# Optimization experiments

Hardware: AMD Instinct MI355X
Metric: run time of the kernel (lower is better)

The kernel has to match this reference:

```python
import jax, jax.numpy as jnp
import numpy as np

B, S, D, E = 2, 2048, 1024, 8
H = 2 * D          # hidden_dim = 2*n_embd
A = H // 16        # adapt_dim


def _ln(x, g, b):
    m = x.mean(-1, keepdims=True)
    v = x.var(-1, keepdims=True)
    return (x - m) * jax.lax.rsqrt(v + 1e-5) * g + b


def setup_inputs() -> dict:
    key = jax.random.key(0)
    ks = jax.random.split(key, 16)
    s = 1.0 / np.sqrt(D)        # shared-linear init scale
    sa = s * 0.01               # adapter-linear init scale
    sg = 0.01 / np.sqrt(A)      # expert adapter init scale
    f32 = jnp.float32
    return {
        "x": jax.random.normal(ks[0], (B, S, D), f32),
        "expert_weights": jax.nn.softmax(jax.random.normal(ks[1], (B * S, E), f32), -1),
        "up_w": jax.random.normal(ks[2], (H, D), f32) * s,
        "gate_w": jax.random.normal(ks[3], (H, D), f32) * s,
        "down_w": jax.random.normal(ks[4], (D, H), f32) * s,
        "pre_w": jax.random.normal(ks[5], (A, D), f32) * sa,
        "post_w": jax.random.normal(ks[6], (A, H), f32) * sa,
        "an_g": jnp.ones((A,), f32),
        "an_b": jnp.zeros((A,), f32),
        "adapt_proj_w": jax.random.normal(ks[7], (H, A), f32) * sa,
        "adapter_w": jax.random.normal(ks[8], (E, A, A), f32) * sg,
        "adapter_g": jnp.ones((E, A), f32),
        "adapter_b": jnp.zeros((E, A), f32),
        "expert_proj_w": jax.random.normal(ks[9], (H, A), f32) * sg,
        "output_proj_w": jax.random.normal(ks[10], (D, H), f32) * sg,
    }


def reference(x, expert_weights, up_w, gate_w, down_w, pre_w, post_w, an_g, an_b,
              adapt_proj_w, adapter_w, adapter_g, adapter_b, expert_proj_w, output_proj_w):
    # ---- SharedExpertMLP ----
    up = x @ up_w.T                                  # [B,S,H]
    gate = x @ gate_w.T                              # [B,S,H]
    hidden = jax.nn.silu(gate) * up                  # SwiGLU
    adapt_in = _ln(x @ pre_w.T, an_g, an_b)          # [B,S,A]
    adapt_out = _ln(hidden @ post_w.T, an_g, an_b)   # [B,S,A]
    w = jnp.einsum('bsa,bta->bst', adapt_in, adapt_out)
    w = jax.nn.silu(jnp.clip(w, -5.0, 5.0))          # clamp+SiLU score
    # explicit fp32 bmm as in original autocast-disabled block
    adapt = jnp.einsum('bst,bta->bsa',
                       w.astype(jnp.float32),
                       adapt_in.astype(jnp.float32)).astype(x.dtype)
    hidden = hidden + 0.1 * (adapt @ adapt_proj_w.T)
    shared_out = hidden @ down_w.T                   # [B,S,D] (dropout is identity in eval)

    # ---- per-token expert mixing ----
    xf = x.reshape(-1, x.shape[-1])                  # [N,D], N=B*S
    a = _ln(xf @ pre_w.T, an_g, an_b)                # [N,A]
    h = jnp.einsum('na,eca->nec', a, adapter_w)      # per-expert low-rank adapt [N,E,A]
    h = _ln(h, adapter_g[None], adapter_b[None])
    mixed = jnp.einsum('ne,nea->na', expert_weights, h)   # combine experts [N,A]
    out = (mixed @ expert_proj_w.T) @ output_proj_w.T     # [N,D]
    return shared_out + out.reshape(x.shape)
```

## Files before the change

kernel.cpp:

```cpp
#include <hip/hip_runtime.h>
#include <hip/hip_bf16.h>
#include <math.h>

#define Bq 2
#define Sq 2048
#define Dq 1024
#define Eq 8
#define Hq 2048
#define Aq 128
#define Nq (Bq*Sq)

typedef __attribute__((ext_vector_type(4))) float f32x4;
typedef __attribute__((ext_vector_type(8))) short bfrag;

__device__ __forceinline__ float silu_f(float x) {
    return x / (1.0f + expf(-x));
}
__device__ __forceinline__ unsigned short f2bf(float x) {
    unsigned u = __float_as_uint(x);
    u += 0x7fffu + ((u >> 16) & 1u);
    return (unsigned short)(u >> 16);
}
__device__ __forceinline__ float bf2f(unsigned short h) {
    return __uint_as_float(((unsigned)h) << 16);
}
__device__ __forceinline__ void gl16(const unsigned short* g, unsigned short* l) {
    __builtin_amdgcn_global_load_lds(
        (const __attribute__((address_space(1))) void*)g,
        (__attribute__((address_space(3))) void*)(void*)l, 16, 0, 0);
}

#define WAITV_BAR(N)                                            \
    asm volatile("s_waitcnt vmcnt(" #N ")" ::: "memory");       \
    __builtin_amdgcn_s_barrier();                               \
    asm volatile("" ::: "memory")
#define END_BAR()                                               \
    asm volatile("" ::: "memory");                              \
    __builtin_amdgcn_s_barrier();                               \
    asm volatile("" ::: "memory")

__global__ __launch_bounds__(256)
void convert_all(const float* __restrict__ x,  const float* __restrict__ gw,
                 const float* __restrict__ uw, const float* __restrict__ dw,
                 const float* __restrict__ pw, const float* __restrict__ ow,
                 const float* __restrict__ opw, const float* __restrict__ aw,
                 const float* __restrict__ apw, const float* __restrict__ epw,
                 unsigned short* xh,  unsigned short* gwh, unsigned short* uwh,
                 unsigned short* dwh, unsigned short* pwh, unsigned short* powh,
                 unsigned short* oph, unsigned short* adw, unsigned short* apT)
{
    __shared__ float t[32][33];
    if (blockIdx.x >= 2048) {
        int bid = blockIdx.x - 2048;
        int z   = bid >> 8;
        int rem = bid & 255;
        int bx  = rem & 3, by = rem >> 2;
        const float* in = z ? epw : apw;
        unsigned short* out = apT + (size_t)z * Hq * Aq;
        int tx = threadIdx.x & 31, ty = threadIdx.x >> 5;
        int r0 = by * 32, c0 = bx * 32;
#pragma unroll
        for (int j = 0; j < 4; j++)
            t[ty + j * 8][tx] = in[(size_t)(r0 + ty + j * 8) * Aq + c0 + tx];
        __syncthreads();
#pragma unroll
        for (int j = 0; j < 4; j++)
            out[(size_t)(c0 + ty + j * 8) * Hq + r0 + tx] = f2bf(t[tx][ty + j * 8]);
        return;
    }
    const int T = 3276800;
    for (int i = blockIdx.x * 256 + threadIdx.x; i < T; i += 2048 * 256) {
        const float* in; unsigned short* hi; int j = i;
        if (j < 1048576)                 { in = x;   hi = xh;  }
        else if ((j -= 1048576) < 524288){ in = gw;  hi = gwh; }
        else if ((j -= 524288) < 524288) { in = uw;  hi = uwh; }
        else if ((j -= 524288) < 524288) { in = dw;  hi = dwh; }
        else if ((j -= 524288) < 32768)  { in = pw;  hi = pwh; }
        else if ((j -= 32768) < 65536)   { in = ow;  hi = powh; }
        else if ((j -= 65536) < 524288)  { in = opw; hi = oph; }
        else { j -= 524288;                in = aw;  hi = adw; }
        float4 v = ((const float4*)in)[j];
        ((ushort4*)hi)[j] = make_ushort4(f2bf(v.x), f2bf(v.y), f2bf(v.z), f2bf(v.w));
    }
}

template<int EPI>
__global__ __launch_bounds__(512)
void mg(const unsigned short* __restrict__ Ah, const unsigned short* __restrict__ Bh,
        void* __restrict__ Cv, int N, int K, int kchunks,
        long zA, long zB, long zC, long pz)
{
    __shared__ __align__(16) unsigned short lds[32768];

    const int tid = threadIdx.x;
    const int l   = tid & 63;
    const int w   = tid >> 6;
    const int wr  = w >> 2, wc = w & 3;
    const int bm0 = blockIdx.y * 128, bn0 = blockIdx.x * 128;
    const int bz  = blockIdx.z / kchunks;
    const int kz  = blockIdx.z - bz * kchunks;
    const int kcnt = K / kchunks;
    const int kbeg = kz * kcnt;
    const int kend = kbeg + kcnt;

    const unsigned short* A0 = Ah + (size_t)bz * zA;
    const unsigned short* B0 = Bh + (size_t)bz * zB;

    const int srow = tid >> 3;
    const int sq   = (tid & 7) ^ (srow & 7);
    const size_t aoff = (size_t)(bm0 + srow) * K + sq * 8;
    const size_t boff = (size_t)(bn0 + srow) * K + sq * 8;
    const size_t r64  = (size_t)64 * K;

    auto stage = [&](int b, int kt) {
        unsigned short* d = &lds[b * 16384 + (w << 9)];
        gl16(A0 + aoff + kt,       d + 0);
        gl16(A0 + aoff + kt + r64, d + 4096);
        gl16(B0 + boff + kt,       d + 8192);
        gl16(B0 + boff + kt + r64, d + 12288);
    };

    const int rowa = (wr * 64 + (l & 15)) * 64;
    const int rowb = (wc * 32 + (l & 15)) * 64;
    const int q0 = (((l >> 4)    ) ^ (l & 7)) << 3;
    const int q1 = (((l >> 4) + 4) ^ (l & 7)) << 3;

    f32x4 acc[4][2];
#pragma unroll
    for (int i = 0; i < 4; i++)
#pragma unroll
        for (int j = 0; j < 2; j++) acc[i][j] = (f32x4){0.f, 0.f, 0.f, 0.f};

    stage(0, kbeg);
    int cur = 0;
    for (int kt = kbeg; kt < kend; kt += 64) {
        if (kt + 64 < kend) {
            stage(cur ^ 1, kt + 64);
            WAITV_BAR(4);
        } else {
            WAITV_BAR(0);
        }
        const int cb = cur * 16384;
#pragma unroll
        for (int ks = 0; ks < 2; ks++) {
            const int qo = ks ? q1 : q0;
            bfrag a4[4], b4[2];
#pragma unroll
            for (int f = 0; f < 4; f++)
                a4[f] = *(const bfrag*)&lds[cb + rowa + f * 1024 + qo];
#pragma unroll
            for (int f = 0; f < 2; f++)
                b4[f] = *(const bfrag*)&lds[cb + 8192 + rowb + f * 1024 + qo];
#pragma unroll
            for (int i = 0; i < 4; i++)
#pragma unroll
                for (int j = 0; j < 2; j++)
                    acc[i][j] = __builtin_amdgcn_mfma_f32_16x16x32_bf16(a4[i], b4[j], acc[i][j], 0, 0, 0);
        }
        END_BAR();
        cur ^= 1;
    }

    const int crow0 = bm0 + wr * 64 + (l >> 4) * 4;
    const int ccol0 = bn0 + wc * 32 + (l & 15);
#pragma unroll
    for (int i = 0; i < 4; i++)
#pragma unroll
        for (int j = 0; j < 2; j++)
#pragma unroll
            for (int r = 0; r < 4; r++) {
                size_t idx = (size_t)(crow0 + i * 16 + r) * N + (ccol0 + j * 16);
                float v = acc[i][j][r];
                if (EPI == 0)
                    ((float*)Cv + (size_t)bz * zC + (size_t)kz * pz)[idx] = v;
                else if (EPI == 1)
                    ((unsigned short*)Cv + (size_t)bz * zC)[idx] =
                        f2bf(silu_f(fminf(fmaxf(v, -5.f), 5.f)));
                else
                    ((unsigned short*)Cv + (size_t)bz * zC)[idx] = f2bf(v);
            }
}

__global__ __launch_bounds__(512)
void gsc(const unsigned short* __restrict__ ainh, const unsigned short* __restrict__ aouth,
         const unsigned short* __restrict__ ainT, float* __restrict__ p3)
{
    __shared__ __align__(16) unsigned short lds[65536];
    const int AIN = 0, AOUT = 16384, AINT = 32768, PB = 49152;

    const int tid = threadIdx.x;
    const int l   = tid & 63;
    const int w   = tid >> 6;
    const int wr  = w >> 2, wc = w & 3;
    const int tz  = blockIdx.x;
    const int ib  = blockIdx.y;
    const int b   = blockIdx.z;
    const long SA = (long)Sq * Aq;

    auto stage32 = [&](int base, const unsigned short* src, size_t kstride) {
#pragma unroll
        for (int rd = 0; rd < 4; rd++) {
            int grow = rd * 32 + (w << 2) + (l >> 4);
            int slot = (l & 15) ^ (grow & 15);
            gl16(src + (size_t)grow * kstride + slot * 8,
                 &lds[base + rd * 4096 + (w << 9)]);
        }
    };

    const unsigned short* ainI_src = ainh + (size_t)b * SA + (size_t)(ib * 128) * Aq;
    f32x4 acc2[4][2];
#pragma unroll
    for (int i = 0; i < 4; i++)
#pragma unroll
        for (int j = 0; j < 2; j++) acc2[i][j] = (f32x4){0.f, 0.f, 0.f, 0.f};

    {
        int tglob = tz * 2;
        stage32(AIN,  ainI_src, Aq);
        stage32(AOUT, aouth + (size_t)b * SA + (size_t)(tglob * 128) * Aq, Aq);
        stage32(AINT, ainT  + (size_t)b * SA + (size_t)(tglob * 128), Sq);
        WAITV_BAR(0);
    }

    const int rowa = (wr * 64 + (l & 15)) * 128;
    const int rowb = (wc * 32 + (l & 15)) * 128;

#pragma unroll 1
    for (int t = 0; t < 2; t++) {
        if (t == 1) {
            int tglob = tz * 2 + 1;
            stage32(AOUT, aouth + (size_t)b * SA + (size_t)(tglob * 128) * Aq, Aq);
            stage32(AINT, ainT  + (size_t)b * SA + (size_t)(tglob * 128), Sq);
            WAITV_BAR(0);
        }
        f32x4 acc1[4][2];
#pragma unroll
        for (int i = 0; i < 4; i++)
#pragma unroll
            for (int j = 0; j < 2; j++) acc1[i][j] = (f32x4){0.f, 0.f, 0.f, 0.f};
#pragma unroll
        for (int ks = 0; ks < 4; ks++) {
            const int qo = ((ks * 4 + (l >> 4)) ^ (l & 15)) << 3;
            bfrag a4[4], b4[2];
#pragma unroll
            for (int f = 0; f < 4; f++)
                a4[f] = *(const bfrag*)&lds[AIN + rowa + f * 2048 + qo];
#pragma unroll
            for (int f = 0; f < 2; f++)
                b4[f] = *(const bfrag*)&lds[AOUT + rowb + f * 2048 + qo];
#pragma unroll
            for (int i = 0; i < 4; i++)
#pragma unroll
                for (int j = 0; j < 2; j++)
                    acc1[i][j] = __builtin_amdgcn_mfma_f32_16x16x32_bf16(a4[i], b4[j], acc1[i][j], 0, 0, 0);
        }
        {
            const int prow0 = wr * 64 + (l >> 4) * 4;
            const int pcol0 = wc * 32 + (l & 15);
#pragma unroll
            for (int i = 0; i < 4; i++)
#pragma unroll
                for (int j = 0; j < 2; j++)
#pragma unroll
                    for (int r = 0; r < 4; r++) {
                        int pr = prow0 + i * 16 + r;
                        int pc = pcol0 + j * 16;
                        float v = silu_f(fminf(fmaxf(acc1[i][j][r], -5.f), 5.f));
                        lds[PB + pr * 128 + (((pc >> 3) ^ (pr & 15)) << 3) + (pc & 7)] = f2bf(v);
                    }
        }
        __syncthreads();
#pragma unroll
        for (int ks = 0; ks < 4; ks++) {
            const int qo = ((ks * 4 + (l >> 4)) ^ (l & 15)) << 3;
            bfrag a4[4], b4[2];
#pragma unroll
            for (int f = 0; f < 4; f++)
                a4[f] = *(const bfrag*)&lds[PB + rowa + f * 2048 + qo];
#pragma unroll
            for (int f = 0; f < 2; f++)
                b4[f] = *(const bfrag*)&lds[AINT + rowb + f * 2048 + qo];
#pragma unroll
            for (int i = 0; i < 4; i++)
#pragma unroll
                for (int j = 0; j < 2; j++)
                    acc2[i][j] = __builtin_amdgcn_mfma_f32_16x16x32_bf16(a4[i], b4[j], acc2[i][j], 0, 0, 0);
        }
        __syncthreads();
    }

    const int crow0 = wr * 64 + (l >> 4) * 4;
    const int ccol0 = wc * 32 + (l & 15);
    float* dst = p3 + ((size_t)(b * 8 + tz) * Sq + ib * 128) * Aq;
#pragma unroll
    for (int i = 0; i < 4; i++)
#pragma unroll
        for (int j = 0; j < 2; j++)
#pragma unroll
            for (int r = 0; r < 4; r++)
                dst[(size_t)(crow0 + i * 16 + r) * Aq + ccol0 + j * 16] = acc2[i][j][r];
}

__global__ __launch_bounds__(512)
void gup(const unsigned short* __restrict__ xh, const unsigned short* __restrict__ gwh,
         const unsigned short* __restrict__ uwh, unsigned short* __restrict__ hh)
{
    __shared__ __align__(16) unsigned short lds[24576];
    const int tid = threadIdx.x;
    const int l   = tid & 63;
    const int w   = tid >> 6;
    const int wr  = w >> 2, wc = w & 3;

    int id  = blockIdx.y * gridDim.x + blockIdx.x;
    int xcd = id & 7, j = id >> 3;
    int bx  = (xcd & 1) * 8 + (j & 7);
    int by  = (xcd >> 1) * 8 + (j >> 3);
    const int bm0 = by * 128, bn0 = bx * 128;

    const int srow = tid >> 2;
    const int sq   = (tid & 3) ^ ((srow >> 1) & 3);
    const size_t aoff = (size_t)(bm0 + srow) * Dq + sq * 8;
    const size_t boff = (size_t)(bn0 + srow) * Dq + sq * 8;

    const int rowa = (wr * 64 + (l & 15)) * 32;
    const int rowb = (wc * 32 + (l & 15)) * 32;
    const int q0 = (((l >> 4)) ^ (((l & 15) >> 1) & 3)) << 3;

    auto stage = [&](int b, int kt) {
        unsigned short* d = &lds[b * 12288 + (w << 9)];
        gl16(xh  + aoff + kt, d + 0);
        gl16(gwh + boff + kt, d + 4096);
        gl16(uwh + boff + kt, d + 8192);
    };

    f32x4 accg[4][2], accu[4][2];
#pragma unroll
    for (int i = 0; i < 4; i++)
#pragma unroll
        for (int jj = 0; jj < 2; jj++) {
            accg[i][jj] = (f32x4){0.f, 0.f, 0.f, 0.f};
            accu[i][jj] = (f32x4){0.f, 0.f, 0.f, 0.f};
        }

    stage(0, 0);
    int cur = 0;
    for (int kt = 0; kt < Dq; kt += 32) {
        if (kt + 32 < Dq) {
            stage(cur ^ 1, kt + 32);
            WAITV_BAR(3);
        } else {
            WAITV_BAR(0);
        }
        const int cb = cur * 12288;
        bfrag a4[4], g4[2], u4[2];
#pragma unroll
        for (int f = 0; f < 4; f++)
            a4[f] = *(const bfrag*)&lds[cb + rowa + f * 512 + q0];
#pragma unroll
        for (int f = 0; f < 2; f++) {
            g4[f] = *(const bfrag*)&lds[cb + 4096 + rowb + f * 512 + q0];
            u4[f] = *(const bfrag*)&lds[cb + 8192 + rowb + f * 512 + q0];
        }
#pragma unroll
        for (int i = 0; i < 4; i++)
#pragma unroll
            for (int jj = 0; jj < 2; jj++) {
                accg[i][jj] = __builtin_amdgcn_mfma_f32_16x16x32_bf16(a4[i], g4[jj], accg[i][jj], 0, 0, 0);
                accu[i][jj] = __builtin_amdgcn_mfma_f32_16x16x32_bf16(a4[i], u4[jj], accu[i][jj], 0, 0, 0);
            }
        END_BAR();
        cur ^= 1;
    }

    const int crow0 = bm0 + wr * 64 + (l >> 4) * 4;
    const int ccol0 = bn0 + wc * 32 + (l & 15);
#pragma unroll
    for (int i = 0; i < 4; i++)
#pragma unroll
        for (int jj = 0; jj < 2; jj++)
#pragma unroll
            for (int r = 0; r < 4; r++) {
                size_t idx = (size_t)(crow0 + i * 16 + r) * Hq + (ccol0 + jj * 16);
                hh[idx] = f2bf(silu_f(accg[i][jj][r]) * accu[i][jj][r]);
            }
}

__global__ __launch_bounds__(512)
void gfinal(const unsigned short* __restrict__ hh, const unsigned short* __restrict__ dwh,
            const unsigned short* __restrict__ acat, const unsigned short* __restrict__ kcat,
            float* __restrict__ out)
{
    __shared__ __align__(16) unsigned short lds[49152];
    const int tid = threadIdx.x;
    const int l   = tid & 63;
    const int w   = tid >> 6;
    const int wr  = w >> 2, wc = w & 3;

    int nb  = gridDim.x * gridDim.y;
    int id  = blockIdx.y * gridDim.x + blockIdx.x;
    int id2 = (id & 7) * (nb >> 3) + (id >> 3);
    int bx  = id2 % gridDim.x, by = id2 / gridDim.x;
    const int bm0 = by * 128, bn0 = bx * 128;

    const int srow = tid >> 3;
    const int sq   = (tid & 7) ^ (srow & 7);
    const int rowa = (wr * 64 + (l & 15)) * 64;
    const int rowb = (wc * 32 + (l & 15)) * 64;
    const int q0 = (((l >> 4)    ) ^ (l & 7)) << 3;
    const int q1 = (((l >> 4) + 4) ^ (l & 7)) << 3;

    f32x4 acc[4][2];
#pragma unroll
    for (int i = 0; i < 4; i++)
#pragma unroll
        for (int j = 0; j < 2; j++) acc[i][j] = (f32x4){0.f, 0.f, 0.f, 0.f};

    {
        const size_t aoff = (size_t)(bm0 + srow) * Hq + sq * 8;
        const size_t boff = (size_t)(bn0 + srow) * Hq + sq * 8;
        const size_t r64  = (size_t)64 * Hq;
        auto stage = [&](int b, int kt) {
            unsigned short* d = &lds[b * 16384 + (w << 9)];
            gl16(hh  + aoff + kt,       d + 0);
            gl16(hh  + aoff + kt + r64, d + 4096);
            gl16(dwh + boff + kt,       d + 8192);
            gl16(dwh + boff + kt + r64, d + 12288);
        };
        stage(0, 0);
        stage(1, 64);
        int cur = 0;
        for (int kt = 0; kt < Hq; kt += 64) {
            if (kt + 64 < Hq) { WAITV_BAR(4); } else { WAITV_BAR(0); }
            if (kt + 128 < Hq) {
                int nb3 = (cur + 2 >= 3) ? cur - 1 : cur + 2;
                stage(nb3, kt + 128);
            }
            const int cb = cur * 16384;
#pragma unroll
            for (int ks = 0; ks < 2; ks++) {
                const int qo = ks ? q1 : q0;
                bfrag a4[4], b4[2];
#pragma unroll
                for (int f = 0; f < 4; f++)
                    a4[f] = *(const bfrag*)&lds[cb + rowa + f * 1024 + qo];
#pragma unroll
                for (int f = 0; f < 2; f++)
                    b4[f] = *(const bfrag*)&lds[cb + 8192 + rowb + f * 1024 + qo];
#pragma unroll
                for (int i = 0; i < 4; i++)
#pragma unroll
                    for (int j = 0; j < 2; j++)
                        acc[i][j] = __builtin_amdgcn_mfma_f32_16x16x32_bf16(a4[i], b4[j], acc[i][j], 0, 0, 0);
            }
            cur = (cur == 2) ? 0 : cur + 1;
        }
    }
    END_BAR();
    {
        const size_t aoff = (size_t)(bm0 + srow) * 256 + sq * 8;
        const size_t boff = (size_t)(bn0 + srow) * 256 + sq * 8;
        const size_t r64  = (size_t)64 * 256;
        auto stage2 = [&](int b, int kt) {
            unsigned short* d = &lds[b * 16384 + (w << 9)];
            gl16(acat + aoff + kt,       d + 0);
            gl16(acat + aoff + kt + r64, d + 4096);
            gl16(kcat + boff + kt,       d + 8192);
            gl16(kcat + boff + kt + r64, d + 12288);
        };
        stage2(0, 0);
        stage2(1, 64);
        int cur = 0;
        for (int kt = 0; kt < 256; kt += 64) {
            if (kt + 64 < 256) { WAITV_BAR(4); } else { WAITV_BAR(0); }
            if (kt + 128 < 256) {
                int nb3 = (cur + 2 >= 3) ? cur - 1 : cur + 2;
                stage2(nb3, kt + 128);
            }
            const int cb = cur * 16384;
#pragma unroll
            for (int ks = 0; ks < 2; ks++) {
                const int qo = ks ? q1 : q0;
                bfrag a4[4], b4[2];
#pragma unroll
                for (int f = 0; f < 4; f++)
                    a4[f] = *(const bfrag*)&lds[cb + rowa + f * 1024 + qo];
#pragma unroll
                for (int f = 0; f < 2; f++)
                    b4[f] = *(const bfrag*)&lds[cb + 8192 + rowb + f * 1024 + qo];
#pragma unroll
                for (int i = 0; i < 4; i++)
#pragma unroll
                    for (int j = 0; j < 2; j++)
                        acc[i][j] = __builtin_amdgcn_mfma_f32_16x16x32_bf16(a4[i], b4[j], acc[i][j], 0, 0, 0);
            }
            cur = (cur == 2) ? 0 : cur + 1;
        }
    }

    const int crow0 = bm0 + wr * 64 + (l >> 4) * 4;
    const int ccol0 = bn0 + wc * 32 + (l & 15);
#pragma unroll
    for (int i = 0; i < 4; i++)
#pragma unroll
        for (int j = 0; j < 2; j++)
#pragma unroll
            for (int r = 0; r < 4; r++)
                out[(size_t)(crow0 + i * 16 + r) * Dq + ccol0 + j * 16] = acc[i][j][r];
}

template<int NZ, bool WT>
__global__ __launch_bounds__(256)
void rln(const float* __restrict__ p, unsigned short* __restrict__ oh,
         unsigned short* __restrict__ aT,
         const float* __restrict__ g, const float* __restrict__ b, long pstride)
{
    int row  = blockIdx.x * 4 + (threadIdx.x >> 6);
    int lane = threadIdx.x & 63;
    long base = (long)row * Aq;
    float x0 = 0.f, x1 = 0.f;
#pragma unroll
    for (int z = 0; z < NZ; z++) {
        x0 += p[base + z * pstride + lane];
        x1 += p[base + z * pstride + lane + 64];
    }
    float s  = x0 + x1;
    float ss = x0 * x0 + x1 * x1;
#pragma unroll
    for (int off = 32; off > 0; off >>= 1) {
        s  += __shfl_xor(s, off);
        ss += __shfl_xor(ss, off);
    }
    float m  = s * (1.0f / Aq);
    float v  = ss * (1.0f / Aq) - m * m;
    float rs = rsqrtf(v + 1e-5f);
    unsigned short h0 = f2bf((x0 - m) * rs * g[lane]      + b[lane]);
    unsigned short h1 = f2bf((x1 - m) * rs * g[lane + 64] + b[lane + 64]);
    oh[base + lane]      = h0;
    oh[base + lane + 64] = h1;
    if (WT) {
        int bb2 = row >> 11, sidx = row & 2047;
        unsigned short* t = aT + (size_t)bb2 * Sq * Aq + sidx;
        t[(size_t)lane * Sq]        = h0;
        t[(size_t)(lane + 64) * Sq] = h1;
    }
}

template<int NZ>
__global__ __launch_bounds__(256)
void rbf(const float* __restrict__ p, unsigned short* __restrict__ o,
         int rowsPerB, float scale, int total, int ostride, int ocol, int ocolStep)
{
    int i = blockIdx.x * 256 + threadIdx.x;
    if (i >= total) return;
    int n = i >> 7, a = i & 127;
    int bz = n / rowsPerB, s = n - bz * rowsPerB;
    long base = ((long)bz * NZ) * rowsPerB * Aq + (long)s * Aq + a;
    float acc = 0.f;
#pragma unroll
    for (int z = 0; z < NZ; z++) acc += p[base + (long)z * rowsPerB * Aq];
    o[(long)s * ostride + (ocol + bz * ocolStep) + a +
      (ocolStep ? 0 : (long)bz * rowsPerB * ostride)] = f2bf(acc * scale);
}

__global__ __launch_bounds__(256)
void tailk(const float* __restrict__ p3, const unsigned short* __restrict__ he,
           const float* __restrict__ ew, const float* __restrict__ g,
           const float* __restrict__ bb, unsigned short* __restrict__ acat)
{
    if (blockIdx.x < 2048) {
        int i = blockIdx.x * 256 + threadIdx.x;
        int n = i >> 7, a = i & 127;
        int bz = n >> 11, s = n & 2047;
        long base = ((long)bz * 8) * Sq * Aq + (long)s * Aq + a;
        float acc = 0.f;
#pragma unroll
        for (int z = 0; z < 8; z++) acc += p3[base + (long)z * Sq * Aq];
        acat[(long)n * 256 + a] = f2bf(acc * 0.1f);
        return;
    }
    int n    = (blockIdx.x - 2048) * 4 + (threadIdx.x >> 6);
    int lane = threadIdx.x & 63;
    float a0 = 0.0f, a1 = 0.0f;
#pragma unroll
    for (int e = 0; e < Eq; e++) {
        const unsigned short* r = he + ((long)e * Nq + n) * Aq;
        float x0 = bf2f(r[lane]), x1 = bf2f(r[lane + 64]);
        float s  = x0 + x1;
        float ss = x0 * x0 + x1 * x1;
#pragma unroll
        for (int off = 32; off > 0; off >>= 1) {
            s  += __shfl_xor(s, off);
            ss += __shfl_xor(ss, off);
        }
        float m  = s * (1.0f / Aq);
        float v  = ss * (1.0f / Aq) - m * m;
        float rs = rsqrtf(v + 1e-5f);
        float wv = ew[(long)n * Eq + e];
        a0 += wv * ((x0 - m) * rs * g[e * Aq + lane]      + bb[e * Aq + lane]);
        a1 += wv * ((x1 - m) * rs * g[e * Aq + lane + 64] + bb[e * Aq + lane + 64]);
    }
    acat[(long)n * 256 + 128 + lane]      = f2bf(a0);
    acat[(long)n * 256 + 128 + lane + 64] = f2bf(a1);
}

extern "C" void kernel_launch(void* const* d_in, const int* in_sizes, int n_in,
                              void* d_out, int out_size, void* d_ws, size_t ws_size,
                              hipStream_t stream)
{
    const float* x             = (const float*)d_in[0];
    const float* ew            = (const float*)d_in[1];
    const float* up_w          = (const float*)d_in[2];
    const float* gate_w        = (const float*)d_in[3];
    const float* down_w        = (const float*)d_in[4];
    const float* pre_w         = (const float*)d_in[5];
    const float* post_w        = (const float*)d_in[6];
    const float* an_g          = (const float*)d_in[7];
    const float* an_b          = (const float*)d_in[8];
    const float* adapt_proj_w  = (const float*)d_in[9];
    const float* adapter_w     = (const float*)d_in[10];
    const float* adapter_g     = (const float*)d_in[11];
    const float* adapter_b     = (const float*)d_in[12];
    const float* expert_proj_w = (const float*)d_in[13];
    const float* output_proj_w = (const float*)d_in[14];
    float* out = (float*)d_out;

#define OFF(kb) ((char*)d_ws + (size_t)(kb) * 1024)
    float* kdp  = (float*)OFF(0);
    float* p1   = (float*)OFF(16384);
    float* p2   = (float*)OFF(0);
    float* p3   = (float*)OFF(0);
    unsigned short* he = (unsigned short*)OFF(16384);
    unsigned short* hh   = (unsigned short*)OFF(32768);
    unsigned short* xh   = (unsigned short*)OFF(49152);
    unsigned short* gwh  = (unsigned short*)OFF(57344);
    unsigned short* uwh  = (unsigned short*)OFF(61440);
    unsigned short* dwh  = (unsigned short*)OFF(65536);
    unsigned short* oph  = (unsigned short*)OFF(69632);
    unsigned short* pwh  = (unsigned short*)OFF(73728);
    unsigned short* powh = (unsigned short*)OFF(73984);
    unsigned short* apT  = (unsigned short*)OFF(74496);
    unsigned short* epT  = (unsigned short*)OFF(75008);
    unsigned short* ainh = (unsigned short*)OFF(75520);
    unsigned short* ainT = (unsigned short*)OFF(76544);
    unsigned short* aouth= (unsigned short*)OFF(77568);
    unsigned short* adw  = (unsigned short*)OFF(78592);
    unsigned short* kcat = (unsigned short*)OFF(78848);
    unsigned short* acat = (unsigned short*)OFF(79360);
#undef OFF
    (void)epT;

    dim3 blk(256), blk512(512);
    const long NA = (long)Nq * Aq;

    convert_all<<<dim3(2560), blk, 0, stream>>>(x, gate_w, up_w, down_w, pre_w,
        post_w, output_proj_w, adapter_w, adapt_proj_w, expert_proj_w,
        xh, gwh, uwh, dwh, pwh, powh, oph, adw, apT);

    mg<0><<<dim3(1, 8, 32), blk512, 0, stream>>>(dwh, apT, kdp, Aq, Hq, 16,
        (long)Dq * Hq, (long)Aq * Hq, (long)16 * Dq * Aq, (long)Dq * Aq);
    rbf<16><<<dim3(1024), blk, 0, stream>>>(kdp, kcat, Dq, 1.0f, 2 * Dq * Aq, 256, 0, 128);

    mg<0><<<dim3(1, 32, 8), blk512, 0, stream>>>(xh, pwh, p1, Aq, Dq, 8, 0, 0, 0, NA);
    rln<8, true><<<dim3(1024), blk, 0, stream>>>(p1, ainh, ainT, an_g, an_b, NA);

    mg<2><<<dim3(1, 32, 8), blk512, 0, stream>>>(ainh, adw, he, Aq, Aq, 1,
        0, (long)Aq * Aq, NA, 0);

    gup<<<dim3(16, 32), blk512, 0, stream>>>(xh, gwh, uwh, hh);

    mg<0><<<dim3(1, 32, 8), blk512, 0, stream>>>(hh, powh, p2, Aq, Hq, 8, 0, 0, 0, NA);
    rln<8, false><<<dim3(1024), blk, 0, stream>>>(p2, aouth, nullptr, an_g, an_b, NA);

    gsc<<<dim3(8, 16, 2), blk512, 0, stream>>>(ainh, aouth, ainT, p3);

    tailk<<<dim3(3072), blk, 0, stream>>>(p3, he, ew, adapter_g, adapter_b, acat);

    gfinal<<<dim3(8, 32), blk512, 0, stream>>>(hh, dwh, acat, kcat, out);
}
```

Before: 163.0 us.

## Enlarge gate/up GEMM tile to 256 rows with K=64 staged sub-pipeline

```diff
diff --git a/kernel.cpp b/kernel.cpp
--- a/kernel.cpp
+++ b/kernel.cpp
@@ -35,6 +35,11 @@
     __builtin_amdgcn_s_barrier();                               \
     asm volatile("" ::: "memory")
 #define END_BAR()                                               \
+    asm volatile("" ::: "memory");                              \
+    __builtin_amdgcn_s_barrier();                               \
+    asm volatile("" ::: "memory")
+#define WAITV(N) asm volatile("s_waitcnt vmcnt(" #N ")" ::: "memory")
+#define BARF()                                                  \
     asm volatile("" ::: "memory");                              \
     __builtin_amdgcn_s_barrier();                               \
     asm volatile("" ::: "memory")
@@ -305,77 +310,119 @@
 void gup(const unsigned short* __restrict__ xh, const unsigned short* __restrict__ gwh,
          const unsigned short* __restrict__ uwh, unsigned short* __restrict__ hh)
 {
-    __shared__ __align__(16) unsigned short lds[24576];
+    __shared__ __align__(16) unsigned short lds[65536];
     const int tid = threadIdx.x;
     const int l   = tid & 63;
     const int w   = tid >> 6;
-    const int wr  = w >> 2, wc = w & 3;
+    const int wr  = w >> 2;
+    const int wc  = w & 3;
 
     int id  = blockIdx.y * gridDim.x + blockIdx.x;
-    int xcd = id & 7, j = id >> 3;
-    int bx  = (xcd & 1) * 8 + (j & 7);
-    int by  = (xcd >> 1) * 8 + (j >> 3);
-    const int bm0 = by * 128, bn0 = bx * 128;
-
-    const int srow = tid >> 2;
-    const int sq   = (tid & 3) ^ ((srow >> 1) & 3);
-    const size_t aoff = (size_t)(bm0 + srow) * Dq + sq * 8;
-    const size_t boff = (size_t)(bn0 + srow) * Dq + sq * 8;
-
-    const int rowa = (wr * 64 + (l & 15)) * 32;
-    const int rowb = (wc * 32 + (l & 15)) * 32;
-    const int q0 = (((l >> 4)) ^ (((l & 15) >> 1) & 3)) << 3;
-
-    auto stage = [&](int b, int kt) {
-        unsigned short* d = &lds[b * 12288 + (w << 9)];
-        gl16(xh  + aoff + kt, d + 0);
-        gl16(gwh + boff + kt, d + 4096);
-        gl16(uwh + boff + kt, d + 8192);
+    int xcd = id & 7, j0 = id >> 3;
+    int bx  = (xcd & 3) * 4 + (j0 & 3);
+    int by  = (xcd >> 2) * 8 + (j0 >> 2);
+    const int bm0 = by * 256, bn0 = bx * 128;
+
+    const int srw = tid >> 3;
+    const int sq  = (tid & 7) ^ (srw & 7);
+    auto stageU = [&](int b, int u, int kt) {
+        unsigned short* d = &lds[b * 32768 + u * 8192 + (tid << 3)];
+        const unsigned short* src = (u < 2) ? xh : (u == 2 ? gwh : uwh);
+        int baserow = (u < 2) ? (bm0 + u * 128) : bn0;
+        size_t o = (size_t)(baserow + srw) * Dq + kt + sq * 8;
+        gl16(src + o,                   d);
+        gl16(src + o + (size_t)64 * Dq, d + 4096);
     };
 
-    f32x4 accg[4][2], accu[4][2];
-#pragma unroll
-    for (int i = 0; i < 4; i++)
+    const int rowa = (wr * 128 + (l & 15)) * 64;
+    const int rowb = (wc * 32  + (l & 15)) * 64;
+    const int q0 = (((l >> 4)    ) ^ (l & 7)) << 3;
+    const int q1 = (((l >> 4) + 4) ^ (l & 7)) << 3;
+
+    f32x4 accg[8][2], accu[8][2];
+#pragma unroll
+    for (int i = 0; i < 8; i++)
 #pragma unroll
         for (int jj = 0; jj < 2; jj++) {
             accg[i][jj] = (f32x4){0.f, 0.f, 0.f, 0.f};
             accu[i][jj] = (f32x4){0.f, 0.f, 0.f, 0.f};
         }
 
-    stage(0, 0);
+    stageU(0, 0, 0); stageU(0, 1, 0); stageU(0, 2, 0); stageU(0, 3, 0);
     int cur = 0;
-    for (int kt = 0; kt < Dq; kt += 32) {
-        if (kt + 32 < Dq) {
-            stage(cur ^ 1, kt + 32);
-            WAITV_BAR(3);
-        } else {
-            WAITV_BAR(0);
-        }
-        const int cb = cur * 12288;
-        bfrag a4[4], g4[2], u4[2];
-#pragma unroll
-        for (int f = 0; f < 4; f++)
-            a4[f] = *(const bfrag*)&lds[cb + rowa + f * 512 + q0];
-#pragma unroll
-        for (int f = 0; f < 2; f++) {
-            g4[f] = *(const bfrag*)&lds[cb + 4096 + rowb + f * 512 + q0];
-            u4[f] = *(const bfrag*)&lds[cb + 8192 + rowb + f * 512 + q0];
-        }
-#pragma unroll
-        for (int i = 0; i < 4; i++)
-#pragma unroll
-            for (int jj = 0; jj < 2; jj++) {
-                accg[i][jj] = __builtin_amdgcn_mfma_f32_16x16x32_bf16(a4[i], g4[jj], accg[i][jj], 0, 0, 0);
-                accu[i][jj] = __builtin_amdgcn_mfma_f32_16x16x32_bf16(a4[i], u4[jj], accu[i][jj], 0, 0, 0);
-            }
-        END_BAR();
-        cur ^= 1;
-    }
-
-    const int crow0 = bm0 + wr * 64 + (l >> 4) * 4;
+    for (int kt = 0; kt < Dq; kt += 64) {
+        const int pf = (kt + 64 < Dq);
+        const int cb = cur * 32768;
+        const int nx = cur ^ 1;
+        bfrag a4[8], b4[2];
+
+        WAITV(2);
+        BARF();
+#pragma unroll
+        for (int f = 0; f < 8; f++)
+            a4[f] = *(const bfrag*)&lds[cb + rowa + f * 1024 + q0];
+#pragma unroll
+        for (int f = 0; f < 2; f++)
+            b4[f] = *(const bfrag*)&lds[cb + 16384 + rowb + f * 1024 + q0];
+        if (pf) stageU(nx, 0, kt + 64);
+        __builtin_amdgcn_s_setprio(1);
+#pragma unroll
+        for (int i = 0; i < 8; i++)
+#pragma unroll
+            for (int jj = 0; jj < 2; jj++)
+                accg[i][jj] = __builtin_amdgcn_mfma_f32_16x16x32_bf16(a4[i], b4[jj], accg[i][jj], 0, 0, 0);
+        __builtin_amdgcn_s_setprio(0);
+
+        if (pf) { WAITV(2); } else { WAITV(0); }
+        BARF();
+#pragma unroll
+        for (int f = 0; f < 2; f++)
+            b4[f] = *(const bfrag*)&lds[cb + 24576 + rowb + f * 1024 + q0];
+        if (pf) stageU(nx, 1, kt + 64);
+        __builtin_amdgcn_s_setprio(1);
+#pragma unroll
+        for (int i = 0; i < 8; i++)
+#pragma unroll
+            for (int jj = 0; jj < 2; jj++)
+                accu[i][jj] = __builtin_amdgcn_mfma_f32_16x16x32_bf16(a4[i], b4[jj], accu[i][jj], 0, 0, 0);
+        __builtin_amdgcn_s_setprio(0);
+
+        BARF();
+#pragma unroll
+        for (int f = 0; f < 8; f++)
+            a4[f] = *(const bfrag*)&lds[cb + rowa + f * 1024 + q1];
+#pragma unroll
+        for (int f = 0; f < 2; f++)
+            b4[f] = *(const bfrag*)&lds[cb + 16384 + rowb + f * 1024 + q1];
+        if (pf) stageU(nx, 2, kt + 64);
+        __builtin_amdgcn_s_setprio(1);
+#pragma unroll
+        for (int i = 0; i < 8; i++)
+#pragma unroll
+            for (int jj = 0; jj < 2; jj++)
+                accg[i][jj] = __builtin_amdgcn_mfma_f32_16x16x32_bf16(a4[i], b4[jj], accg[i][jj], 0, 0, 0);
+        __builtin_amdgcn_s_setprio(0);
+
+        BARF();
+#pragma unroll
+        for (int f = 0; f < 2; f++)
+            b4[f] = *(const bfrag*)&lds[cb + 24576 + rowb + f * 1024 + q1];
+        if (pf) stageU(nx, 3, kt + 64);
+        __builtin_amdgcn_s_setprio(1);
+#pragma unroll
+        for (int i = 0; i < 8; i++)
+#pragma unroll
+            for (int jj = 0; jj < 2; jj++)
+                accu[i][jj] = __builtin_amdgcn_mfma_f32_16x16x32_bf16(a4[i], b4[jj], accu[i][jj], 0, 0, 0);
+        __builtin_amdgcn_s_setprio(0);
+
+        cur = nx;
+    }
+
+    const int crow0 = bm0 + wr * 128 + (l >> 4) * 4;
     const int ccol0 = bn0 + wc * 32 + (l & 15);
 #pragma unroll
-    for (int i = 0; i < 4; i++)
+    for (int i = 0; i < 8; i++)
 #pragma unroll
         for (int jj = 0; jj < 2; jj++)
 #pragma unroll
@@ -666,7 +713,7 @@
     mg<2><<<dim3(1, 32, 8), blk512, 0, stream>>>(ainh, adw, he, Aq, Aq, 1,
         0, (long)Aq * Aq, NA, 0);
 
-    gup<<<dim3(16, 32), blk512, 0, stream>>>(xh, gwh, uwh, hh);
+    gup<<<dim3(16, 16), blk512, 0, stream>>>(xh, gwh, uwh, hh);
 
     mg<0><<<dim3(1, 32, 8), blk512, 0, stream>>>(hh, powh, p2, Aq, Hq, 8, 0, 0, 0, NA);
     rln<8, false><<<dim3(1024), blk, 0, stream>>>(p2, aouth, nullptr, an_g, an_b, NA);
```

Result: faster. 159.8 us (-2.0%).
